# Performance work log

Measured on AMD Instinct MI355X. Metric: run time of the kernel, lower is better.

The kernel has to match this reference:

```python
import jax, jax.numpy as jnp
import numpy as np

N, E, F_IN, H = 50000, 800000, 16, 128
EPS = 1e-5


def bn(x, gamma, beta):
    # training-mode batchnorm over node dim
    mu = jnp.mean(x, axis=0)
    var = jnp.var(x, axis=0)
    return (x - mu) * jax.lax.rsqrt(var + EPS) * gamma + beta


def gat_conv(x, src, dst, W, att_src, att_dst, bias, heads, out_dim, n):
    h = (x @ W).reshape(n, heads, out_dim)              # [N,H,D]
    a_src = jnp.sum(h * att_src, axis=-1)               # [N,H]
    a_dst = jnp.sum(h * att_dst, axis=-1)               # [N,H]
    e = jax.nn.leaky_relu(a_src[src] + a_dst[dst], 0.2) # [E,H]
    e_max = jax.ops.segment_max(e, dst, num_segments=n)
    e = jnp.exp(e - e_max[dst])
    denom = jax.ops.segment_sum(e, dst, num_segments=n)
    alpha = e / (denom[dst] + 1e-16)                     # [E,H]
    msg = h[src] * alpha[:, :, None]                     # [E,H,D]
    out = jax.ops.segment_sum(msg, dst, num_segments=n)
    return out.reshape(n, heads * out_dim) + bias


def setup_inputs() -> dict:
    key = jax.random.key(0)
    ks = jax.random.split(key, 20)
    s = lambda i, shape, sc=0.05: jax.random.normal(ks[i], shape, jnp.float32) * sc
    inp = {
        "x": jax.random.normal(ks[0], (N, F_IN), jnp.float32),
        "edge_index": jax.random.randint(ks[1], (2, E), 0, N, jnp.int32),
        "W_in": s(2, (F_IN, H)), "b_in": jnp.zeros((H,), jnp.float32),
        "g0": jnp.ones((H,), jnp.float32), "be0": jnp.zeros((H,), jnp.float32),
        "W1": s(3, (H, 2 * H)), "as1": s(4, (2, H)), "ad1": s(5, (2, H)),
        "bias1": jnp.zeros((2 * H,), jnp.float32),
        "g1": jnp.ones((2 * H,), jnp.float32), "be1": jnp.zeros((2 * H,), jnp.float32),
        "W2": s(6, (2 * H, H)), "as2": s(7, (1, H)), "ad2": s(8, (1, H)),
        "bias2": jnp.zeros((H,), jnp.float32),
        "g2": jnp.ones((H,), jnp.float32), "be2": jnp.zeros((H,), jnp.float32),
        "Wf1": s(9, (H, H // 2)), "bf1": jnp.zeros((H // 2,), jnp.float32),
        "gf": jnp.ones((H // 2,), jnp.float32), "bef": jnp.zeros((H // 2,), jnp.float32),
        "Wf2": s(10, (H // 2, 1)), "bf2": jnp.zeros((1,), jnp.float32),
    }
    return inp


def reference(x, edge_index, W_in, b_in, g0, be0, W1, as1, ad1, bias1, g1, be1,
              W2, as2, ad2, bias2, g2, be2, Wf1, bf1, gf, bef, Wf2, bf2):
    n = x.shape[0]
    # PyG GATConv adds self loops by default
    loops = jnp.arange(n, dtype=edge_index.dtype)
    src = jnp.concatenate([edge_index[0], loops])
    dst = jnp.concatenate([edge_index[1], loops])

    h = jax.nn.relu(bn(x @ W_in + b_in, g0, be0))
    h = jax.nn.relu(bn(gat_conv(h, src, dst, W1, as1, ad1, bias1, 2, H, n), g1, be1))
    h = jax.nn.relu(bn(gat_conv(h, src, dst, W2, as2, ad2, bias2, 1, H, n), g2, be2))
    h = jax.nn.relu(bn(h @ Wf1 + bf1, gf, bef))
    # dropout: identity in eval
    return jnp.squeeze(h @ Wf2 + bf2, axis=-1)
```

## Files before the change

kernel.cpp:

```cpp
#include <hip/hip_runtime.h>
#include <hip/hip_bf16.h>


__device__ inline float bf2f(unsigned short u) {
    return __uint_as_float(((unsigned)u) << 16);
}

template<bool BF16OUT>
__global__ __launch_bounds__(256) void gemm_f32(
    const float* __restrict__ A, const float* __restrict__ B,
    const float* __restrict__ bias, void* __restrict__ Cout,
    int M, int Nc, int K)
{
    __shared__ float As[16][68];
    __shared__ float Bs[16][68];
    const int t  = threadIdx.x;
    const int m0 = blockIdx.x * 64;
    const int n0 = blockIdx.y * 64;
    const int tx = t & 15;
    const int ty = t >> 4;
    const int lar = t >> 2;
    const int lac = (t & 3) * 4;
    const int lbr = t >> 4;
    const int lbc = (t & 15) * 4;

    float acc[4][4] = {};
    for (int k0 = 0; k0 < K; k0 += 16) {
        {
            int gr = m0 + lar;
            float4 v = make_float4(0.f, 0.f, 0.f, 0.f);
            if (gr < M) v = *reinterpret_cast<const float4*>(A + (size_t)gr * K + k0 + lac);
            As[lac + 0][lar] = v.x; As[lac + 1][lar] = v.y;
            As[lac + 2][lar] = v.z; As[lac + 3][lar] = v.w;
        }
        {
            float4 v = *reinterpret_cast<const float4*>(B + (size_t)(k0 + lbr) * Nc + n0 + lbc);
            *reinterpret_cast<float4*>(&Bs[lbr][lbc]) = v;
        }
        __syncthreads();
#pragma unroll
        for (int kk = 0; kk < 16; ++kk) {
            float a[4], b[4];
            *reinterpret_cast<float4*>(a) = *reinterpret_cast<const float4*>(&As[kk][ty * 4]);
            *reinterpret_cast<float4*>(b) = *reinterpret_cast<const float4*>(&Bs[kk][tx * 4]);
#pragma unroll
            for (int i = 0; i < 4; ++i)
#pragma unroll
                for (int j = 0; j < 4; ++j)
                    acc[i][j] = fmaf(a[i], b[j], acc[i][j]);
        }
        __syncthreads();
    }
    float bj[4] = {0.f, 0.f, 0.f, 0.f};
    if (bias) *reinterpret_cast<float4*>(bj) = *reinterpret_cast<const float4*>(bias + n0 + tx * 4);
#pragma unroll
    for (int i = 0; i < 4; ++i) {
        int row = m0 + ty * 4 + i;
        if (row < M) {
            float v0 = acc[i][0] + bj[0], v1 = acc[i][1] + bj[1];
            float v2 = acc[i][2] + bj[2], v3 = acc[i][3] + bj[3];
            if constexpr (BF16OUT) {
                __hip_bfloat16 h[4];
                h[0] = __float2bfloat16(v0); h[1] = __float2bfloat16(v1);
                h[2] = __float2bfloat16(v2); h[3] = __float2bfloat16(v3);
                *reinterpret_cast<uint2*>((__hip_bfloat16*)Cout + (size_t)row * Nc + n0 + tx * 4) =
                    *reinterpret_cast<uint2*>(h);
            } else {
                *reinterpret_cast<float4*>((float*)Cout + (size_t)row * Nc + n0 + tx * 4) =
                    make_float4(v0, v1, v2, v3);
            }
        }
    }
}

template<int C>
__global__ __launch_bounds__(256) void bn_stats(const float* __restrict__ y,
                                                double* __restrict__ sums, int Nn)
{
    constexpr int R = (256 / C) < 1 ? 1 : (256 / C);
    const int t = threadIdx.x;
    const int col = (C >= 256) ? t : (t % C);
    const int r0  = (C >= 256) ? 0 : (t / C);
    double s = 0.0, s2 = 0.0;
    for (int row = blockIdx.x * R + r0; row < Nn; row += gridDim.x * R) {
        float v = y[(size_t)row * C + col];
        s += v; s2 += (double)v * (double)v;
    }
    __shared__ double ls[256], ls2[256];
    ls[t] = s; ls2[t] = s2;
    __syncthreads();
    if (t < C) {
#pragma unroll
        for (int k = 1; k < R; ++k) { s += ls[t + k * C]; s2 += ls2[t + k * C]; }
        atomicAdd(&sums[col], s);
        atomicAdd(&sums[C + col], s2);
    }
}

template<int C>
__global__ void bn_fin(const double* __restrict__ sums, const float* __restrict__ g,
                       const float* __restrict__ be, float* __restrict__ sc,
                       float* __restrict__ sh, int Nn)
{
    int c = threadIdx.x;
    if (c < C) {
        double mean = sums[c] / Nn;
        double var  = sums[C + c] / Nn - mean * mean;
        if (var < 0.0) var = 0.0;
        double s = (double)g[c] / sqrt(var + 1e-5);
        sc[c] = (float)s;
        sh[c] = (float)((double)be[c] - mean * s);
    }
}

template<int C>
__global__ __launch_bounds__(256) void bn_apply_relu(float* __restrict__ y,
                                                     const float* __restrict__ sc,
                                                     const float* __restrict__ sh, int total4)
{
    int i = blockIdx.x * blockDim.x + threadIdx.x;
    int stride = gridDim.x * blockDim.x;
    for (; i < total4; i += stride) {
        float4 v = reinterpret_cast<float4*>(y)[i];
        int cb = (i * 4) % C;
        float4 s = *reinterpret_cast<const float4*>(sc + cb);
        float4 h = *reinterpret_cast<const float4*>(sh + cb);
        v.x = fmaxf(fmaf(v.x, s.x, h.x), 0.f);
        v.y = fmaxf(fmaf(v.y, s.y, h.y), 0.f);
        v.z = fmaxf(fmaf(v.z, s.z, h.z), 0.f);
        v.w = fmaxf(fmaf(v.w, s.w, h.w), 0.f);
        reinterpret_cast<float4*>(y)[i] = v;
    }
}

template<int HEADS>
__global__ __launch_bounds__(256) void att_scores(
    const __hip_bfloat16* __restrict__ g, const float* __restrict__ att_s,
    const float* __restrict__ att_d, float* __restrict__ a_s,
    float* __restrict__ a_d, int Nn)
{
    constexpr int C = HEADS * 128;
    constexpr int VEC = C / 64;
    constexpr int GROUP = 128 / VEC;
    int wid  = (blockIdx.x * 256 + threadIdx.x) >> 6;
    int lane = threadIdx.x & 63;
    if (wid >= Nn) return;
    float ps = 0.f, pd = 0.f;
    const __hip_bfloat16* gp = g + (size_t)wid * C + lane * VEC;
    unsigned short u[VEC];
    if constexpr (VEC == 4) *reinterpret_cast<uint2*>(u) = *reinterpret_cast<const uint2*>(gp);
    else                    *reinterpret_cast<unsigned*>(u) = *reinterpret_cast<const unsigned*>(gp);
#pragma unroll
    for (int j = 0; j < VEC; ++j) {
        float v = bf2f(u[j]);
        ps += v * att_s[lane * VEC + j];
        pd += v * att_d[lane * VEC + j];
    }
    for (int off = 1; off < GROUP; off <<= 1) {
        ps += __shfl_xor(ps, off, 64);
        pd += __shfl_xor(pd, off, 64);
    }
    if ((lane & (GROUP - 1)) == 0) {
        int head = (lane * VEC) >> 7;
        a_s[wid * HEADS + head] = ps;
        a_d[wid * HEADS + head] = pd;
    }
}

__global__ void count_edges(const int* __restrict__ ei, int E, int Nn, int* __restrict__ counts)
{
    int k = blockIdx.x * blockDim.x + threadIdx.x;
    if (k >= E + Nn) return;
    int d = (k < E) ? ei[E + k] : (k - E);
    atomicAdd(&counts[d], 1);
}

__global__ void scan_chunk_sum(const int* __restrict__ counts, int Nn, int* __restrict__ csum)
{
    __shared__ int sh[256];
    int i = blockIdx.x * 256 + threadIdx.x;
    sh[threadIdx.x] = (i < Nn) ? counts[i] : 0;
    __syncthreads();
    for (int off = 128; off > 0; off >>= 1) {
        if (threadIdx.x < off) sh[threadIdx.x] += sh[threadIdx.x + off];
        __syncthreads();
    }
    if (threadIdx.x == 0) csum[blockIdx.x] = sh[0];
}

__global__ void scan_chunks(const int* __restrict__ csum, int nchunks, int* __restrict__ coff,
                            int* __restrict__ offsets, int Nn, int Etot)
{
    __shared__ int sh[256];
    int t = threadIdx.x;
    int v = (t < nchunks) ? csum[t] : 0;
    sh[t] = v;
    __syncthreads();
    for (int off = 1; off < 256; off <<= 1) {
        int add = (t >= off) ? sh[t - off] : 0;
        __syncthreads();
        sh[t] += add;
        __syncthreads();
    }
    if (t < nchunks) coff[t] = sh[t] - v;
    if (t == 0) offsets[Nn] = Etot;
}

__global__ void scan_final(const int* __restrict__ counts, int Nn,
                           const int* __restrict__ coff, int* __restrict__ offsets)
{
    __shared__ int sh[256];
    int t = threadIdx.x;
    int i = blockIdx.x * 256 + t;
    int v = (i < Nn) ? counts[i] : 0;
    sh[t] = v;
    __syncthreads();
    for (int off = 1; off < 256; off <<= 1) {
        int add = (t >= off) ? sh[t - off] : 0;
        __syncthreads();
        sh[t] += add;
        __syncthreads();
    }
    if (i < Nn) offsets[i] = coff[blockIdx.x] + sh[t] - v;
}

__global__ void scatter_edges(const int* __restrict__ ei, int E, int Nn,
                              const int* __restrict__ offsets, int* __restrict__ cursor,
                              int* __restrict__ csr_src)
{
    int k = blockIdx.x * blockDim.x + threadIdx.x;
    if (k >= E + Nn) return;
    int s, d;
    if (k < E) { s = ei[k]; d = ei[E + k]; } else { s = k - E; d = k - E; }
    int pos = offsets[d] + atomicAdd(&cursor[d], 1);
    csr_src[pos] = s;
}

template<int C, int HEADS>
__global__ __launch_bounds__(256) void gat_agg_fused(
    const __hip_bfloat16* __restrict__ hfeat,
    const float* __restrict__ a_s, const float* __restrict__ a_d,
    const int* __restrict__ offsets, const int* __restrict__ csr_src,
    const float* __restrict__ bias, float* __restrict__ out, int Nn)
{
    constexpr int VEC = C / 64;
    int wid  = (blockIdx.x * 256 + threadIdx.x) >> 6;
    int lane = threadIdx.x & 63;
    if (wid >= Nn) return;
    const int head = (HEADS == 1) ? 0 : (lane >> 5);
    const int beg = offsets[wid], end = offsets[wid + 1];

    float ad0 = a_d[wid * HEADS + 0];
    float ad1 = (HEADS == 2) ? a_d[wid * HEADS + 1] : 0.f;
    const float adh = (head == 0) ? ad0 : ad1;

    float m0 = -1e30f, m1 = -1e30f;
    for (int p = beg + lane; p < end; p += 64) {
        int s = csr_src[p];
        {
            float e = a_s[s * HEADS + 0] + ad0;
            e = (e > 0.f) ? e : 0.2f * e;
            m0 = fmaxf(m0, e);
        }
        if (HEADS == 2) {
            float e = a_s[s * HEADS + 1] + ad1;
            e = (e > 0.f) ? e : 0.2f * e;
            m1 = fmaxf(m1, e);
        }
    }
    for (int off = 1; off < 64; off <<= 1) {
        m0 = fmaxf(m0, __shfl_xor(m0, off, 64));
        if (HEADS == 2) m1 = fmaxf(m1, __shfl_xor(m1, off, 64));
    }
    const float mh = (head == 0) ? m0 : m1;

    float acc[VEC] = {};
    float wsum = 0.f;
    for (int p = beg; p < end; ++p) {
        int s = csr_src[p];
        float e = a_s[s * HEADS + head] + adh;
        e = (e > 0.f) ? e : 0.2f * e;
        float w = expf(e - mh);
        wsum += w;
        const __hip_bfloat16* hp = hfeat + (size_t)s * C + lane * VEC;
        if constexpr (VEC == 4) {
            uint2 d = *reinterpret_cast<const uint2*>(hp);
            acc[0] = fmaf(w, bf2f((unsigned short)(d.x & 0xffff)), acc[0]);
            acc[1] = fmaf(w, bf2f((unsigned short)(d.x >> 16)),    acc[1]);
            acc[2] = fmaf(w, bf2f((unsigned short)(d.y & 0xffff)), acc[2]);
            acc[3] = fmaf(w, bf2f((unsigned short)(d.y >> 16)),    acc[3]);
        } else {
            unsigned d = *reinterpret_cast<const unsigned*>(hp);
            acc[0] = fmaf(w, bf2f((unsigned short)(d & 0xffff)), acc[0]);
            acc[1] = fmaf(w, bf2f((unsigned short)(d >> 16)),    acc[1]);
        }
    }
    float inv = 1.f / (wsum + 1e-16f);
    float* op = out + (size_t)wid * C + lane * VEC;
    if constexpr (VEC == 4) {
        *reinterpret_cast<float4*>(op) = make_float4(
            fmaf(acc[0], inv, bias[lane * 4 + 0]), fmaf(acc[1], inv, bias[lane * 4 + 1]),
            fmaf(acc[2], inv, bias[lane * 4 + 2]), fmaf(acc[3], inv, bias[lane * 4 + 3]));
    } else {
        *reinterpret_cast<float2*>(op) = make_float2(
            fmaf(acc[0], inv, bias[lane * 2 + 0]), fmaf(acc[1], inv, bias[lane * 2 + 1]));
    }
}

__global__ __launch_bounds__(256) void final_dot(const float* __restrict__ h3,
                                                 const float* __restrict__ w,
                                                 const float* __restrict__ b,
                                                 float* __restrict__ out, int Nn)
{
    int wid  = (blockIdx.x * 256 + threadIdx.x) >> 6;
    int lane = threadIdx.x & 63;
    if (wid >= Nn) return;
    float v = h3[(size_t)wid * 64 + lane] * w[lane];
    for (int off = 32; off > 0; off >>= 1) v += __shfl_xor(v, off, 64);
    if (lane == 0) out[wid] = v + b[0];
}

extern "C" void kernel_launch(void* const* d_in, const int* in_sizes, int n_in,
                              void* d_out, int out_size, void* d_ws, size_t ws_size,
                              hipStream_t stream)
{
    const float* x     = (const float*)d_in[0];
    const int*   ei    = (const int*)d_in[1];
    const float* W_in  = (const float*)d_in[2];
    const float* b_in  = (const float*)d_in[3];
    const float* g0    = (const float*)d_in[4];
    const float* be0   = (const float*)d_in[5];
    const float* W1    = (const float*)d_in[6];
    const float* as1   = (const float*)d_in[7];
    const float* ad1   = (const float*)d_in[8];
    const float* bias1 = (const float*)d_in[9];
    const float* g1    = (const float*)d_in[10];
    const float* be1   = (const float*)d_in[11];
    const float* W2    = (const float*)d_in[12];
    const float* as2   = (const float*)d_in[13];
    const float* ad2   = (const float*)d_in[14];
    const float* bias2 = (const float*)d_in[15];
    const float* g2    = (const float*)d_in[16];
    const float* be2   = (const float*)d_in[17];
    const float* Wf1   = (const float*)d_in[18];
    const float* bf1   = (const float*)d_in[19];
    const float* gf    = (const float*)d_in[20];
    const float* bef   = (const float*)d_in[21];
    const float* Wf2   = (const float*)d_in[22];
    const float* bf2   = (const float*)d_in[23];

    const int N    = in_sizes[0] / 16;
    const int E    = in_sizes[1] / 2;
    const int Etot = E + N;

    char* ws = (char*)d_ws;
    size_t off = 0;
    auto alloc = [&](size_t bytes) {
        size_t o = off;
        off += (bytes + 255) & ~(size_t)255;
        return o;
    };
    float* buf0 = (float*)(ws + alloc((size_t)N * 128 * 4));
    float* buf2 = (float*)(ws + alloc((size_t)N * 256 * 4));
    float* buf1 = (float*)(ws + alloc((size_t)N * 64 * 4));
    __hip_bfloat16* gbuf = (__hip_bfloat16*)(ws + alloc((size_t)N * 256 * 2));
    float* a_s  = (float*)(ws + alloc((size_t)N * 2 * 4));
    float* a_d  = (float*)(ws + alloc((size_t)N * 2 * 4));
    int* offsets  = (int*)(ws + alloc((size_t)(N + 1) * 4));
    int* csr_src  = (int*)(ws + alloc((size_t)Etot * 4));
    int* csum     = (int*)(ws + alloc(256 * 4));
    int* coff     = (int*)(ws + alloc(256 * 4));
    float* scale  = (float*)(ws + alloc(256 * 4));
    float* shift  = (float*)(ws + alloc(256 * 4));
    size_t zone0 = off;
    int* counts      = (int*)(ws + alloc((size_t)N * 4));
    int* cursor      = (int*)(ws + alloc((size_t)N * 4));
    double* sums0    = (double*)(ws + alloc(2 * 128 * 8));
    double* sums1    = (double*)(ws + alloc(2 * 256 * 8));
    double* sums2    = (double*)(ws + alloc(2 * 128 * 8));
    double* sums3    = (double*)(ws + alloc(2 * 64 * 8));
    size_t zone_bytes = off - zone0;

    hipMemsetAsync(ws + zone0, 0, zone_bytes, stream);

    dim3 blk(256);
    const int gM  = (N + 63) / 64;
    const int gE  = (Etot + 255) / 256;
    const int gW  = (N + 3) / 4;
    const int nch = (N + 255) / 256;

    gemm_f32<false><<<dim3(gM, 2), blk, 0, stream>>>(x, W_in, b_in, buf0, N, 128, 16);
    bn_stats<128><<<dim3(400), blk, 0, stream>>>(buf0, sums0, N);
    bn_fin<128><<<1, 128, 0, stream>>>(sums0, g0, be0, scale, shift, N);
    bn_apply_relu<128><<<dim3(2048), blk, 0, stream>>>(buf0, scale, shift, N * 128 / 4);

    count_edges<<<gE, blk, 0, stream>>>(ei, E, N, counts);
    scan_chunk_sum<<<nch, blk, 0, stream>>>(counts, N, csum);
    scan_chunks<<<1, blk, 0, stream>>>(csum, nch, coff, offsets, N, Etot);
    scan_final<<<nch, blk, 0, stream>>>(counts, N, coff, offsets);
    scatter_edges<<<gE, blk, 0, stream>>>(ei, E, N, offsets, cursor, csr_src);

    gemm_f32<true><<<dim3(gM, 4), blk, 0, stream>>>(buf0, W1, nullptr, gbuf, N, 256, 128);
    att_scores<2><<<dim3(gW), blk, 0, stream>>>(gbuf, as1, ad1, a_s, a_d, N);
    gat_agg_fused<256, 2><<<dim3(gW), blk, 0, stream>>>(gbuf, a_s, a_d, offsets, csr_src, bias1, buf2, N);
    bn_stats<256><<<dim3(400), blk, 0, stream>>>(buf2, sums1, N);
    bn_fin<256><<<1, 256, 0, stream>>>(sums1, g1, be1, scale, shift, N);
    bn_apply_relu<256><<<dim3(2048), blk, 0, stream>>>(buf2, scale, shift, N * 256 / 4);

    gemm_f32<true><<<dim3(gM, 2), blk, 0, stream>>>(buf2, W2, nullptr, gbuf, N, 128, 256);
    att_scores<1><<<dim3(gW), blk, 0, stream>>>(gbuf, as2, ad2, a_s, a_d, N);
    gat_agg_fused<128, 1><<<dim3(gW), blk, 0, stream>>>(gbuf, a_s, a_d, offsets, csr_src, bias2, buf0, N);
    bn_stats<128><<<dim3(400), blk, 0, stream>>>(buf0, sums2, N);
    bn_fin<128><<<1, 128, 0, stream>>>(sums2, g2, be2, scale, shift, N);
    bn_apply_relu<128><<<dim3(2048), blk, 0, stream>>>(buf0, scale, shift, N * 128 / 4);

    gemm_f32<false><<<dim3(gM, 1), blk, 0, stream>>>(buf0, Wf1, bf1, buf1, N, 64, 128);
    bn_stats<64><<<dim3(400), blk, 0, stream>>>(buf1, sums3, N);
    bn_fin<64><<<1, 64, 0, stream>>>(sums3, gf, bef, scale, shift, N);
    bn_apply_relu<64><<<dim3(2048), blk, 0, stream>>>(buf1, scale, shift, N * 64 / 4);

    final_dot<<<dim3(gW), blk, 0, stream>>>(buf1, Wf2, bf2, (float*)d_out, N);
}
```

Before: 709.6 us.

## Process four edges per wavefront concurrently in GAT aggregation with 16B loads

The GAT aggregation kernel now splits each 64-lane wavefront into four 16-lane groups. Each group handles a different incoming edge, and each lane loads 8 bf16 values per head with a 16-byte vector load. Partial sums are combined across groups with shuffles at the end. The aim is more memory-level parallelism and fewer serial loop iterations per node on the gather-bound aggregation, at the cost of more registers, an extra cross-group reduction, and idle lanes when a node's degree is not a multiple of four. It also switches expf to __expf.

Measured after the change: 622.5 us. 1.14x faster.

```diff
diff --git a/kernel.cpp b/kernel.cpp
--- a/kernel.cpp
+++ b/kernel.cpp
@@ -243,67 +243,98 @@
     const int* __restrict__ offsets, const int* __restrict__ csr_src,
     const float* __restrict__ bias, float* __restrict__ out, int Nn)
 {
-    constexpr int VEC = C / 64;
     int wid  = (blockIdx.x * 256 + threadIdx.x) >> 6;
     int lane = threadIdx.x & 63;
     if (wid >= Nn) return;
-    const int head = (HEADS == 1) ? 0 : (lane >> 5);
+    const int gid = lane >> 4;
+    const int gl  = lane & 15;
     const int beg = offsets[wid], end = offsets[wid + 1];
 
-    float ad0 = a_d[wid * HEADS + 0];
-    float ad1 = (HEADS == 2) ? a_d[wid * HEADS + 1] : 0.f;
-    const float adh = (head == 0) ? ad0 : ad1;
-
-    float m0 = -1e30f, m1 = -1e30f;
+    float ad[HEADS];
+#pragma unroll
+    for (int h = 0; h < HEADS; ++h) ad[h] = a_d[wid * HEADS + h];
+
+    float m[HEADS];
+#pragma unroll
+    for (int h = 0; h < HEADS; ++h) m[h] = -1e30f;
     for (int p = beg + lane; p < end; p += 64) {
         int s = csr_src[p];
-        {
-            float e = a_s[s * HEADS + 0] + ad0;
+#pragma unroll
+        for (int h = 0; h < HEADS; ++h) {
+            float e = a_s[s * HEADS + h] + ad[h];
             e = (e > 0.f) ? e : 0.2f * e;
-            m0 = fmaxf(m0, e);
-        }
-        if (HEADS == 2) {
-            float e = a_s[s * HEADS + 1] + ad1;
+            m[h] = fmaxf(m[h], e);
+        }
+    }
+    for (int off = 1; off < 64; off <<= 1) {
+#pragma unroll
+        for (int h = 0; h < HEADS; ++h) m[h] = fmaxf(m[h], __shfl_xor(m[h], off, 64));
+    }
+
+    float acc[HEADS][8];
+#pragma unroll
+    for (int h = 0; h < HEADS; ++h)
+#pragma unroll
+        for (int j = 0; j < 8; ++j) acc[h][j] = 0.f;
+    float wsum[HEADS];
+#pragma unroll
+    for (int h = 0; h < HEADS; ++h) wsum[h] = 0.f;
+
+    for (int p0 = beg; p0 < end; p0 += 4) {
+        int p = p0 + gid;
+        bool act = (p < end);
+        int s = csr_src[act ? p : beg];
+        float w[HEADS];
+#pragma unroll
+        for (int h = 0; h < HEADS; ++h) {
+            float e = a_s[s * HEADS + h] + ad[h];
             e = (e > 0.f) ? e : 0.2f * e;
-            m1 = fmaxf(m1, e);
-        }
-    }
-    for (int off = 1; off < 64; off <<= 1) {
-        m0 = fmaxf(m0, __shfl_xor(m0, off, 64));
-        if (HEADS == 2) m1 = fmaxf(m1, __shfl_xor(m1, off, 64));
-    }
-    const float mh = (head == 0) ? m0 : m1;
-
-    float acc[VEC] = {};
-    float wsum = 0.f;
-    for (int p = beg; p < end; ++p) {
-        int s = csr_src[p];
-        float e = a_s[s * HEADS + head] + adh;
-        e = (e > 0.f) ? e : 0.2f * e;
-        float w = expf(e - mh);
-        wsum += w;
-        const __hip_bfloat16* hp = hfeat + (size_t)s * C + lane * VEC;
-        if constexpr (VEC == 4) {
-            uint2 d = *reinterpret_cast<const uint2*>(hp);
-            acc[0] = fmaf(w, bf2f((unsigned short)(d.x & 0xffff)), acc[0]);
-            acc[1] = fmaf(w, bf2f((unsigned short)(d.x >> 16)),    acc[1]);
-            acc[2] = fmaf(w, bf2f((unsigned short)(d.y & 0xffff)), acc[2]);
-            acc[3] = fmaf(w, bf2f((unsigned short)(d.y >> 16)),    acc[3]);
-        } else {
-            unsigned d = *reinterpret_cast<const unsigned*>(hp);
-            acc[0] = fmaf(w, bf2f((unsigned short)(d & 0xffff)), acc[0]);
-            acc[1] = fmaf(w, bf2f((unsigned short)(d >> 16)),    acc[1]);
-        }
-    }
-    float inv = 1.f / (wsum + 1e-16f);
-    float* op = out + (size_t)wid * C + lane * VEC;
-    if constexpr (VEC == 4) {
-        *reinterpret_cast<float4*>(op) = make_float4(
-            fmaf(acc[0], inv, bias[lane * 4 + 0]), fmaf(acc[1], inv, bias[lane * 4 + 1]),
-            fmaf(acc[2], inv, bias[lane * 4 + 2]), fmaf(acc[3], inv, bias[lane * 4 + 3]));
-    } else {
-        *reinterpret_cast<float2*>(op) = make_float2(
-            fmaf(acc[0], inv, bias[lane * 2 + 0]), fmaf(acc[1], inv, bias[lane * 2 + 1]));
+            w[h] = act ? __expf(e - m[h]) : 0.f;
+            wsum[h] += w[h];
+        }
+        if (act) {
+            const __hip_bfloat16* row = hfeat + (size_t)s * C;
+#pragma unroll
+            for (int h = 0; h < HEADS; ++h) {
+                uint4 d = *reinterpret_cast<const uint4*>(row + h * 128 + gl * 8);
+                float wh = w[h];
+                acc[h][0] = fmaf(wh, bf2f((unsigned short)(d.x & 0xffff)), acc[h][0]);
+                acc[h][1] = fmaf(wh, bf2f((unsigned short)(d.x >> 16)),    acc[h][1]);
+                acc[h][2] = fmaf(wh, bf2f((unsigned short)(d.y & 0xffff)), acc[h][2]);
+                acc[h][3] = fmaf(wh, bf2f((unsigned short)(d.y >> 16)),    acc[h][3]);
+                acc[h][4] = fmaf(wh, bf2f((unsigned short)(d.z & 0xffff)), acc[h][4]);
+                acc[h][5] = fmaf(wh, bf2f((unsigned short)(d.z >> 16)),    acc[h][5]);
+                acc[h][6] = fmaf(wh, bf2f((unsigned short)(d.w & 0xffff)), acc[h][6]);
+                acc[h][7] = fmaf(wh, bf2f((unsigned short)(d.w >> 16)),    acc[h][7]);
+            }
+        }
+    }
+
+#pragma unroll
+    for (int off = 16; off < 64; off <<= 1) {
+#pragma unroll
+        for (int h = 0; h < HEADS; ++h) {
+            wsum[h] += __shfl_xor(wsum[h], off, 64);
+#pragma unroll
+            for (int j = 0; j < 8; ++j) acc[h][j] += __shfl_xor(acc[h][j], off, 64);
+        }
+    }
+
+    if (gid == 0) {
+        float* op = out + (size_t)wid * C;
+#pragma unroll
+        for (int h = 0; h < HEADS; ++h) {
+            float inv = 1.f / (wsum[h] + 1e-16f);
+            const float* bp = bias + h * 128 + gl * 8;
+            float4 v0 = make_float4(
+                fmaf(acc[h][0], inv, bp[0]), fmaf(acc[h][1], inv, bp[1]),
+                fmaf(acc[h][2], inv, bp[2]), fmaf(acc[h][3], inv, bp[3]));
+            float4 v1 = make_float4(
+                fmaf(acc[h][4], inv, bp[4]), fmaf(acc[h][5], inv, bp[5]),
+                fmaf(acc[h][6], inv, bp[6]), fmaf(acc[h][7], inv, bp[7]));
+            *reinterpret_cast<float4*>(op + h * 128 + gl * 8)     = v0;
+            *reinterpret_cast<float4*>(op + h * 128 + gl * 8 + 4) = v1;
+        }
     }
 }
 
```
